# Kernel optimization log

Hardware: AMD Instinct MI355X
Metric: run time of the kernel (lower is better)

The kernel has to match this reference:

```python
import jax, jax.numpy as jnp
import numpy as np

J, H, MAXREL = 24, 8, 49  # num_joints, temporal heads, max_relative_position


def _pos_encoding(seq_len, d_model):
    pos = jnp.arange(seq_len, dtype=jnp.float32)[:, None]
    i = jnp.arange(d_model, dtype=jnp.float32)[None, :]
    angle = pos / jnp.power(10000.0, 2.0 * jnp.floor(i / 2.0) / d_model)
    return jnp.where(jnp.arange(d_model)[None, :] % 2 == 0, jnp.sin(angle), jnp.cos(angle))  # [S, D]


def _rel_index(seq_len):
    r = jnp.arange(seq_len)
    dist = jnp.clip(r[None, :] - r[:, None], -MAXREL, MAXREL) + MAXREL
    return dist  # [S, S] int


def setup_inputs() -> dict:
    key = jax.random.key(0)
    ks = jax.random.split(key, 12)
    B, S, D = 32, 120, 128
    depth = D // H
    s = 0.02
    x = jax.random.normal(ks[0], (B, S, J, D), dtype=jnp.float32)
    mask = jnp.triu(jnp.ones((1, 1, S, S), dtype=jnp.float32), k=1)  # look-ahead mask
    Wq = jax.random.normal(ks[1], (J, D, D), dtype=jnp.float32) * s
    bq = jnp.zeros((J, D), dtype=jnp.float32)
    Wk = jax.random.normal(ks[2], (J, D, D), dtype=jnp.float32) * s
    bk = jnp.zeros((J, D), dtype=jnp.float32)
    Wv = jax.random.normal(ks[3], (J, D, D), dtype=jnp.float32) * s
    bv = jnp.zeros((J, D), dtype=jnp.float32)
    Wo = jax.random.normal(ks[4], (D, D), dtype=jnp.float32) * s
    bo = jnp.zeros((D,), dtype=jnp.float32)
    key_table = jax.random.normal(ks[5], (2 * MAXREL + 1, depth), dtype=jnp.float32) * s
    val_table = jax.random.normal(ks[6], (2 * MAXREL + 1, depth), dtype=jnp.float32) * s
    return {"x": x, "mask": mask, "Wq": Wq, "bq": bq, "Wk": Wk, "bk": bk,
            "Wv": Wv, "bv": bv, "Wo": Wo, "bo": bo,
            "key_table": key_table, "val_table": val_table}


def reference(x, mask, Wq, bq, Wk, bk, Wv, bv, Wo, bo, key_table, val_table):
    B, S, _, D = x.shape
    depth = D // H
    # absolute positional encoding, broadcast over batch and joints
    x = x + _pos_encoding(S, D)[None, :, None, :]
    xj = jnp.transpose(x, (2, 0, 1, 3))  # [J, B, S, D]
    # per-joint linear projections (torch Linear: y = x @ W^T + b)
    q = jnp.einsum('jbsd,jed->jbse', xj, Wq) + bq[:, None, None, :]
    k = jnp.einsum('jbsd,jed->jbse', xj, Wk) + bk[:, None, None, :]
    v = jnp.einsum('jbsd,jed->jbse', xj, Wv) + bv[:, None, None, :]
    # split heads -> [J, B, H, S, depth]
    split = lambda t: t.reshape(J, B, S, H, depth).transpose(0, 1, 3, 2, 4)
    q, k, v = split(q), split(k), split(v)
    # relative key/value embeddings [S, S, depth]
    rel = _rel_index(S)
    rk = key_table[rel]
    rv = val_table[rel]
    logits = jnp.einsum('jbhsd,jbhtd->jbhst', q, k) + jnp.einsum('jbhsd,std->jbhst', q, rk)
    logits = logits / jnp.float32(np.sqrt(depth)) + mask * (-1e9)
    w = jax.nn.softmax(logits, axis=-1)  # [J, B, H, S, T]
    out = jnp.einsum('jbhst,jbhtd->jbhsd', w, v) + jnp.einsum('jbhst,std->jbhsd', w, rv)
    out = out.transpose(0, 1, 3, 2, 4).reshape(J, B, S, D)  # merge heads
    out = jnp.einsum('jbsd,ed->jbse', out, Wo) + bo  # shared output projection
    outputs = out.transpose(1, 2, 0, 3)  # [B, S, J, D]
    attn_weights = w[..., -1, :].transpose(1, 0, 2, 3)  # [B, J, H, T]
    return outputs, attn_weights
```

## Files before the change

kernel.cpp:

```cpp
#include <hip/hip_runtime.h>
#include <math.h>

#define Jn 24
#define Bn 32
#define Sn 120
#define Dn 128
#define Hn 8
#define DEP 16
#define JC 6
#define NCHUNK 4
#define ALD 136

typedef short bf16x8 __attribute__((ext_vector_type(8)));
typedef float f32x4 __attribute__((ext_vector_type(4)));

__device__ __forceinline__ unsigned short f2b(float f) {
    union { float f; unsigned u; } v; v.f = f;
    unsigned r = v.u + 0x7FFFu + ((v.u >> 16) & 1u);
    return (unsigned short)(r >> 16);
}
__device__ __forceinline__ float b2f(unsigned u16) {
    union { unsigned u; float f; } v; v.u = u16 << 16;
    return v.f;
}

__global__ void pe_kernel(float* __restrict__ pe) {
    const int s = blockIdx.x, d = threadIdx.x;
    const float expo = (float)(2 * (d >> 1)) / (float)Dn;
    const float base = powf(10000.0f, -expo);
    const float ang = (float)s * base;
    pe[s * Dn + d] = (d & 1) ? cosf(ang) : sinf(ang);
}

__global__ __launch_bounds__(256)
void qkv_gemm(const float* __restrict__ x, const float* __restrict__ pe,
              const float* __restrict__ Wq, const float* __restrict__ bq,
              const float* __restrict__ Wk, const float* __restrict__ bk,
              const float* __restrict__ Wv, const float* __restrict__ bv,
              unsigned short* __restrict__ qg, unsigned short* __restrict__ kg,
              unsigned short* __restrict__ vg, int jbase)
{
    extern __shared__ unsigned short lsu[];
    unsigned short* As = lsu;
    unsigned short* Bs = lsu + 128 * ALD;

    const int bid = blockIdx.x;
    const int nt = bid % 3;
    const int mt = (bid / 3) % 30;
    const int jc = bid / 90;
    const int j = jbase + jc;
    const int tid = threadIdx.x;

    const float* Wsel = (nt == 0 ? Wq : (nt == 1 ? Wk : Wv)) + (size_t)j * Dn * Dn;
    const float* bsel = (nt == 0 ? bq : (nt == 1 ? bk : bv)) + (size_t)j * Dn;
    unsigned short* obuf = (nt == 0 ? qg : (nt == 1 ? kg : vg));

    for (int idx = tid; idx < 128 * 32; idx += 256) {
        const int r = idx >> 5;
        const int c = (idx & 31) << 2;
        const int mflat = mt * 128 + r;
        const int b = mflat / Sn;
        const int s = mflat % Sn;
        const float4 xv = *(const float4*)(x + (((size_t)(b * Sn + s)) * Jn + j) * Dn + c);
        const float4 pv = *(const float4*)(pe + s * Dn + c);
        unsigned short* dst = As + r * ALD + c;
        dst[0] = f2b(xv.x + pv.x); dst[1] = f2b(xv.y + pv.y);
        dst[2] = f2b(xv.z + pv.z); dst[3] = f2b(xv.w + pv.w);
    }
    for (int idx = tid; idx < 128 * 32; idx += 256) {
        const int e = idx >> 5;
        const int c = (idx & 31) << 2;
        const float4 wv = *(const float4*)(Wsel + (size_t)e * Dn + c);
        unsigned short* dst = Bs + e * ALD + c;
        dst[0] = f2b(wv.x); dst[1] = f2b(wv.y); dst[2] = f2b(wv.z); dst[3] = f2b(wv.w);
    }
    __syncthreads();

    const int wid = tid >> 6;
    const int lane = tid & 63;
    const int wm = wid >> 1, wn = wid & 1;
    const int g = lane >> 4, q16 = lane & 15;

    f32x4 acc[4][4];
    #pragma unroll
    for (int a = 0; a < 4; ++a)
        #pragma unroll
        for (int c2 = 0; c2 < 4; ++c2) acc[a][c2] = (f32x4){0.f, 0.f, 0.f, 0.f};

    #pragma unroll
    for (int ks = 0; ks < 4; ++ks) {
        const int kof = ks * 32 + g * 8;
        bf16x8 av[4], bvf[4];
        #pragma unroll
        for (int fr = 0; fr < 4; ++fr)
            av[fr] = *(const bf16x8*)(As + (wm * 64 + fr * 16 + q16) * ALD + kof);
        #pragma unroll
        for (int fc = 0; fc < 4; ++fc)
            bvf[fc] = *(const bf16x8*)(Bs + (wn * 64 + fc * 16 + q16) * ALD + kof);
        #pragma unroll
        for (int fr = 0; fr < 4; ++fr)
            #pragma unroll
            for (int fc = 0; fc < 4; ++fc)
                acc[fr][fc] = __builtin_amdgcn_mfma_f32_16x16x32_bf16(av[fr], bvf[fc], acc[fr][fc], 0, 0, 0);
    }

    #pragma unroll
    for (int fc = 0; fc < 4; ++fc) {
        const int e = wn * 64 + fc * 16 + q16;
        const float be = bsel[e];
        const int h = e >> 4, ed = e & 15;
        #pragma unroll
        for (int fr = 0; fr < 4; ++fr) {
            #pragma unroll
            for (int r = 0; r < 4; ++r) {
                const int mflat = mt * 128 + wm * 64 + fr * 16 + g * 4 + r;
                const int b = mflat / Sn, s = mflat % Sn;
                obuf[((size_t)((jc * Bn + b) * Hn + h)) * (Sn * DEP) + s * DEP + ed] =
                    f2b(acc[fr][fc][r] + be);
            }
        }
    }
}

#define A_VCT  0
#define A_RKT  6400
#define A_ABUF 9472
#define A_QRB  35072
#define A_BYTES 43776

__global__ __launch_bounds__(256)
void attn_mfma(const unsigned short* __restrict__ qg, const unsigned short* __restrict__ kg,
               const unsigned short* __restrict__ vg,
               const float* __restrict__ ktab, const float* __restrict__ vtab,
               unsigned short* __restrict__ out_pre, float* __restrict__ attn_w, int jbase)
{
    extern __shared__ char smc[];
    unsigned short* vct = (unsigned short*)(smc + A_VCT);
    unsigned short* rkt = (unsigned short*)(smc + A_RKT);

    const int tid = threadIdx.x;
    const int wid = tid >> 6;
    const int lane = tid & 63;
    const int l15 = lane & 15;
    const int g = lane >> 4;
    const int bh = blockIdx.x;
    const int jc = bh >> 8;
    const int b = (bh >> 3) & 31;
    const int h = bh & 7;
    const int j = jbase + jc;

    unsigned short* ab = (unsigned short*)(smc + A_ABUF) + wid * 16 * 200;
    _Float16*      qrb = (_Float16*)(smc + A_QRB) + wid * 16 * 68;

    {
        unsigned* z = (unsigned*)smc;
        for (int idx = tid; idx < A_BYTES / 4; idx += 256) z[idx] = 0;
    }
    __syncthreads();
    const unsigned* vs = (const unsigned*)vg + (size_t)bh * 960;
    for (int idx = tid; idx < 960; idx += 256) {
        const int s = idx >> 3, ep = idx & 7;
        const unsigned u = vs[idx];
        vct[(2 * ep) * 200 + s] = (unsigned short)(u & 0xffffu);
        vct[(2 * ep + 1) * 200 + s] = (unsigned short)(u >> 16);
    }
    for (int idx = tid; idx < 800; idx += 256) {
        const int d = idx >> 4, e = idx & 15;
        vct[e * 200 + 128 + d] = f2b(vtab[d * DEP + e]);
    }
    for (int idx = tid; idx < 800; idx += 256) {
        const int d = idx >> 4, e = idx & 15;
        rkt[d * 24 + e] = f2b(ktab[d * DEP + e]);
    }
    __syncthreads();

    const unsigned short* qgu = qg + (size_t)bh * 1920;
    const unsigned short* kgu = kg + (size_t)bh * 1920;

    const bf16x8 zf = {0, 0, 0, 0, 0, 0, 0, 0};
    const f32x4 z4 = {0.f, 0.f, 0.f, 0.f};

    #pragma unroll
    for (int half = 0; half < 2; ++half) {
        const int m = half ? (7 - wid) : wid;

        const bf16x8 afr = (g < 2) ? *(const bf16x8*)(qgu + (16 * m + l15) * 16 + g * 8) : zf;
        f32x4 qr[4];
        #pragma unroll
        for (int n = 0; n < 4; ++n) {
            const bf16x8 bfr = (g < 2) ? *(const bf16x8*)(rkt + (16 * n + l15) * 24 + g * 8) : zf;
            qr[n] = __builtin_amdgcn_mfma_f32_16x16x32_bf16(afr, bfr, z4, 0, 0, 0);
        }
        f32x4 acc[8];
        #pragma unroll
        for (int n = 0; n < 8; ++n) {
            if (n > m) break;
            const bf16x8 bfr = (g < 2) ? *(const bf16x8*)(kgu + (16 * n + l15) * 16 + g * 8) : zf;
            acc[n] = __builtin_amdgcn_mfma_f32_16x16x32_bf16(afr, bfr, z4, 0, 0, 0);
        }
        #pragma unroll
        for (int n = 0; n < 4; ++n)
            #pragma unroll
            for (int r = 0; r < 4; ++r)
                qrb[(g * 4 + r) * 68 + 16 * n + l15] = (_Float16)qr[n][r];

        float rs[4];
        #pragma unroll
        for (int r = 0; r < 4; ++r) {
            const int srow = 16 * m + g * 4 + r;
            float pv[8];
            float tot = 0.f, far = 0.f;
            #pragma unroll
            for (int n = 0; n < 8; ++n) {
                if (n > m) break;
                const int t = 16 * n + l15;
                const int dd = t - srow;
                const int dist = (dd <= -49) ? 0 : dd + 49;
                const float qrv = (float)qrb[(g * 4 + r) * 68 + dist];
                float p = 0.f;
                if (t <= srow) p = __expf((acc[n][r] + qrv) * 0.25f);
                pv[n] = p;
                tot += p;
                if (dd <= -49) far += p;
            }
            #pragma unroll
            for (int mk = 1; mk < 16; mk <<= 1) {
                tot += __shfl_xor(tot, mk);
                far += __shfl_xor(far, mk);
            }
            rs[r] = tot;
            const float inv = 1.f / tot;
            #pragma unroll
            for (int n = 0; n < 8; ++n) {
                if (n > m) break;
                const int t = 16 * n + l15;
                const int dd = t - srow;
                ab[(g * 4 + r) * 200 + 16 * n + l15] = f2b(pv[n]);
                if (dd >= -48 && dd <= 0)
                    ab[(g * 4 + r) * 200 + 128 + dd + 49] = f2b(pv[n]);
                if (srow == Sn - 1 && t < Sn)
                    attn_w[(((size_t)(b * Jn + j)) * Hn + h) * Sn + t] = pv[n] * inv;
            }
            if (l15 == 0)
                ab[(g * 4 + r) * 200 + 128 + 0] = f2b(far);
        }

        f32x4 oacc = z4;
        #pragma unroll
        for (int kt = 0; kt < 4; ++kt) {
            if (kt > (m >> 1)) break;
            const bf16x8 aw = *(const bf16x8*)(ab + l15 * 200 + kt * 32 + g * 8);
            const bf16x8 bv = *(const bf16x8*)(vct + l15 * 200 + kt * 32 + g * 8);
            oacc = __builtin_amdgcn_mfma_f32_16x16x32_bf16(aw, bv, oacc, 0, 0, 0);
        }
        #pragma unroll
        for (int kt = 4; kt < 6; ++kt) {
            const bf16x8 aw = *(const bf16x8*)(ab + l15 * 200 + kt * 32 + g * 8);
            const bf16x8 bv = *(const bf16x8*)(vct + l15 * 200 + kt * 32 + g * 8);
            oacc = __builtin_amdgcn_mfma_f32_16x16x32_bf16(aw, bv, oacc, 0, 0, 0);
        }
        #pragma unroll
        for (int r = 0; r < 4; ++r) {
            const int srow = 16 * m + g * 4 + r;
            if (srow < Sn)
                out_pre[((size_t)((j * Bn + b) * Sn) + srow) * Dn + h * DEP + l15] =
                    f2b(oacc[r] / rs[r]);
        }
    }
}

__global__ __launch_bounds__(256)
void oproj_gemm(const unsigned short* __restrict__ Ain, const float* __restrict__ Wo,
                const float* __restrict__ bo, float* __restrict__ out)
{
    extern __shared__ unsigned short lsu[];
    unsigned short* As = lsu;
    unsigned short* Bs = lsu + 128 * ALD;
    const int tid = threadIdx.x;
    const int mt = blockIdx.x;

    for (int idx = tid; idx < 128 * 16; idx += 256) {
        const int r = idx >> 4;
        const int c = (idx & 15) << 3;
        *(uint4*)(As + r * ALD + c) = *(const uint4*)(Ain + ((size_t)(mt * 128 + r)) * Dn + c);
    }
    for (int idx = tid; idx < 128 * 32; idx += 256) {
        const int e = idx >> 5;
        const int c = (idx & 31) << 2;
        const float4 wv = *(const float4*)(Wo + (size_t)e * Dn + c);
        unsigned short* dst = Bs + e * ALD + c;
        dst[0] = f2b(wv.x); dst[1] = f2b(wv.y); dst[2] = f2b(wv.z); dst[3] = f2b(wv.w);
    }
    __syncthreads();

    const int wid = tid >> 6;
    const int lane = tid & 63;
    const int wm = wid >> 1, wn = wid & 1;
    const int g = lane >> 4, q16 = lane & 15;

    f32x4 acc[4][4];
    #pragma unroll
    for (int a = 0; a < 4; ++a)
        #pragma unroll
        for (int c2 = 0; c2 < 4; ++c2) acc[a][c2] = (f32x4){0.f, 0.f, 0.f, 0.f};

    #pragma unroll
    for (int ks = 0; ks < 4; ++ks) {
        const int kof = ks * 32 + g * 8;
        bf16x8 av[4], bvf[4];
        #pragma unroll
        for (int fr = 0; fr < 4; ++fr)
            av[fr] = *(const bf16x8*)(As + (wm * 64 + fr * 16 + q16) * ALD + kof);
        #pragma unroll
        for (int fc = 0; fc < 4; ++fc)
            bvf[fc] = *(const bf16x8*)(Bs + (wn * 64 + fc * 16 + q16) * ALD + kof);
        #pragma unroll
        for (int fr = 0; fr < 4; ++fr)
            #pragma unroll
            for (int fc = 0; fc < 4; ++fc)
                acc[fr][fc] = __builtin_amdgcn_mfma_f32_16x16x32_bf16(av[fr], bvf[fc], acc[fr][fc], 0, 0, 0);
    }

    #pragma unroll
    for (int fc = 0; fc < 4; ++fc) {
        const int e = wn * 64 + fc * 16 + q16;
        const float be = bo[e];
        #pragma unroll
        for (int fr = 0; fr < 4; ++fr) {
            #pragma unroll
            for (int r = 0; r < 4; ++r) {
                const int m = mt * 128 + wm * 64 + fr * 16 + g * 4 + r;
                const int jj = m / (Bn * Sn);
                const int rem = m % (Bn * Sn);
                const int bb = rem / Sn, ss = rem % Sn;
                out[((size_t)(bb * Sn + ss) * Jn + jj) * Dn + e] = acc[fr][fc][r] + be;
            }
        }
    }
}

extern "C" void kernel_launch(void* const* d_in, const int* in_sizes, int n_in,
                              void* d_out, int out_size, void* d_ws, size_t ws_size,
                              hipStream_t stream)
{
    const float* x    = (const float*)d_in[0];
    const float* Wq   = (const float*)d_in[2];
    const float* bq   = (const float*)d_in[3];
    const float* Wk   = (const float*)d_in[4];
    const float* bk   = (const float*)d_in[5];
    const float* Wv   = (const float*)d_in[6];
    const float* bv   = (const float*)d_in[7];
    const float* Wo   = (const float*)d_in[8];
    const float* bo   = (const float*)d_in[9];
    const float* ktab = (const float*)d_in[10];
    const float* vtab = (const float*)d_in[11];

    float* out    = (float*)d_out;
    float* attn_w = out + (size_t)Bn * Sn * Jn * Dn;

    float* pe = (float*)d_ws;
    char* base = (char*)d_ws;
    const size_t csz = (size_t)JC * Bn * Hn * Sn * DEP;
    unsigned short* qg = (unsigned short*)(base + 65536);
    unsigned short* kg = qg + csz;
    unsigned short* vg = kg + csz;
    unsigned short* out_pre = vg + csz;

    pe_kernel<<<Sn, Dn, 0, stream>>>(pe);
    const int gemm_lds = 2 * 128 * ALD * 2;
    for (int c = 0; c < NCHUNK; ++c) {
        qkv_gemm<<<JC * 30 * 3, 256, gemm_lds, stream>>>(
            x, pe, Wq, bq, Wk, bk, Wv, bv, qg, kg, vg, c * JC);
        attn_mfma<<<JC * Bn * Hn, 256, A_BYTES, stream>>>(
            qg, kg, vg, ktab, vtab, out_pre, attn_w, c * JC);
    }
    oproj_gemm<<<(Jn * Bn * Sn) / 128, 256, gemm_lds, stream>>>(out_pre, Wo, bo, out);
}
```

Measured before the change: 267.2 us.

## Reuse the x tile across Q/K/V, fold softmax scale into Q, single-chunk launch

The QKV GEMM now loads and converts each x tile once and loops over the three weight matrices, instead of launching three blocks that each reload it. Q is prescaled by log2(e)/sqrt(depth) so the softmax can use a raw exp2. The far-distance relative-value bucket is handled by subtracting table row 0 and adding it back after normalisation, which removes the 'far' sum and its shuffles. When the workspace is large enough, all 24 joints run in one qkv/attn launch pair instead of four chunks. The cost is that each GEMM block runs serially over three weights with extra barriers, and the larger Q/K/V buffers need more workspace.

```diff
diff --git a/kernel.cpp b/kernel.cpp
--- a/kernel.cpp
+++ b/kernel.cpp
@@ -7,12 +7,18 @@
 #define Dn 128
 #define Hn 8
 #define DEP 16
-#define JC 6
-#define NCHUNK 4
 #define ALD 136
+
+#define QSCL 0.36067376022224085f
 
 typedef short bf16x8 __attribute__((ext_vector_type(8)));
 typedef float f32x4 __attribute__((ext_vector_type(4)));
+
+#if __has_builtin(__builtin_amdgcn_exp2f)
+#define EXP2(x) __builtin_amdgcn_exp2f(x)
+#else
+#define EXP2(x) exp2f(x)
+#endif
 
 __device__ __forceinline__ unsigned short f2b(float f) {
     union { float f; unsigned u; } v; v.f = f;
@@ -45,15 +51,10 @@
     unsigned short* Bs = lsu + 128 * ALD;
 
     const int bid = blockIdx.x;
-    const int nt = bid % 3;
-    const int mt = (bid / 3) % 30;
-    const int jc = bid / 90;
+    const int mt = bid % 30;
+    const int jc = bid / 30;
     const int j = jbase + jc;
     const int tid = threadIdx.x;
-
-    const float* Wsel = (nt == 0 ? Wq : (nt == 1 ? Wk : Wv)) + (size_t)j * Dn * Dn;
-    const float* bsel = (nt == 0 ? bq : (nt == 1 ? bk : bv)) + (size_t)j * Dn;
-    unsigned short* obuf = (nt == 0 ? qg : (nt == 1 ? kg : vg));
 
     for (int idx = tid; idx < 128 * 32; idx += 256) {
         const int r = idx >> 5;
@@ -67,56 +68,65 @@
         dst[0] = f2b(xv.x + pv.x); dst[1] = f2b(xv.y + pv.y);
         dst[2] = f2b(xv.z + pv.z); dst[3] = f2b(xv.w + pv.w);
     }
-    for (int idx = tid; idx < 128 * 32; idx += 256) {
-        const int e = idx >> 5;
-        const int c = (idx & 31) << 2;
-        const float4 wv = *(const float4*)(Wsel + (size_t)e * Dn + c);
-        unsigned short* dst = Bs + e * ALD + c;
-        dst[0] = f2b(wv.x); dst[1] = f2b(wv.y); dst[2] = f2b(wv.z); dst[3] = f2b(wv.w);
-    }
-    __syncthreads();
 
     const int wid = tid >> 6;
     const int lane = tid & 63;
     const int wm = wid >> 1, wn = wid & 1;
     const int g = lane >> 4, q16 = lane & 15;
 
-    f32x4 acc[4][4];
-    #pragma unroll
-    for (int a = 0; a < 4; ++a)
-        #pragma unroll
-        for (int c2 = 0; c2 < 4; ++c2) acc[a][c2] = (f32x4){0.f, 0.f, 0.f, 0.f};
-
-    #pragma unroll
-    for (int ks = 0; ks < 4; ++ks) {
-        const int kof = ks * 32 + g * 8;
-        bf16x8 av[4], bvf[4];
-        #pragma unroll
-        for (int fr = 0; fr < 4; ++fr)
-            av[fr] = *(const bf16x8*)(As + (wm * 64 + fr * 16 + q16) * ALD + kof);
-        #pragma unroll
-        for (int fc = 0; fc < 4; ++fc)
-            bvf[fc] = *(const bf16x8*)(Bs + (wn * 64 + fc * 16 + q16) * ALD + kof);
-        #pragma unroll
-        for (int fr = 0; fr < 4; ++fr)
+    for (int nt = 0; nt < 3; ++nt) {
+        const float* Wsel = (nt == 0 ? Wq : (nt == 1 ? Wk : Wv)) + (size_t)j * Dn * Dn;
+        const float* bsel = (nt == 0 ? bq : (nt == 1 ? bk : bv)) + (size_t)j * Dn;
+        unsigned short* obuf = (nt == 0 ? qg : (nt == 1 ? kg : vg));
+        const float scl = (nt == 0) ? QSCL : 1.0f;
+
+        if (nt) __syncthreads();
+        for (int idx = tid; idx < 128 * 32; idx += 256) {
+            const int e = idx >> 5;
+            const int c = (idx & 31) << 2;
+            const float4 wv = *(const float4*)(Wsel + (size_t)e * Dn + c);
+            unsigned short* dst = Bs + e * ALD + c;
+            dst[0] = f2b(wv.x); dst[1] = f2b(wv.y); dst[2] = f2b(wv.z); dst[3] = f2b(wv.w);
+        }
+        __syncthreads();
+
+        f32x4 acc[4][4];
+        #pragma unroll
+        for (int a = 0; a < 4; ++a)
+            #pragma unroll
+            for (int c2 = 0; c2 < 4; ++c2) acc[a][c2] = (f32x4){0.f, 0.f, 0.f, 0.f};
+
+        #pragma unroll
+        for (int ks = 0; ks < 4; ++ks) {
+            const int kof = ks * 32 + g * 8;
+            bf16x8 av[4], bvf[4];
+            #pragma unroll
+            for (int fr = 0; fr < 4; ++fr)
+                av[fr] = *(const bf16x8*)(As + (wm * 64 + fr * 16 + q16) * ALD + kof);
             #pragma unroll
             for (int fc = 0; fc < 4; ++fc)
-                acc[fr][fc] = __builtin_amdgcn_mfma_f32_16x16x32_bf16(av[fr], bvf[fc], acc[fr][fc], 0, 0, 0);
-    }
-
-    #pragma unroll
-    for (int fc = 0; fc < 4; ++fc) {
-        const int e = wn * 64 + fc * 16 + q16;
-        const float be = bsel[e];
-        const int h = e >> 4, ed = e & 15;
-        #pragma unroll
-        for (int fr = 0; fr < 4; ++fr) {
-            #pragma unroll
-            for (int r = 0; r < 4; ++r) {
-                const int mflat = mt * 128 + wm * 64 + fr * 16 + g * 4 + r;
-                const int b = mflat / Sn, s = mflat % Sn;
-                obuf[((size_t)((jc * Bn + b) * Hn + h)) * (Sn * DEP) + s * DEP + ed] =
-                    f2b(acc[fr][fc][r] + be);
+                bvf[fc] = *(const bf16x8*)(Bs + (wn * 64 + fc * 16 + q16) * ALD + kof);
+            #pragma unroll
+            for (int fr = 0; fr < 4; ++fr)
+                #pragma unroll
+                for (int fc = 0; fc < 4; ++fc)
+                    acc[fr][fc] = __builtin_amdgcn_mfma_f32_16x16x32_bf16(av[fr], bvf[fc], acc[fr][fc], 0, 0, 0);
+        }
+
+        #pragma unroll
+        for (int fc = 0; fc < 4; ++fc) {
+            const int e = wn * 64 + fc * 16 + q16;
+            const float be = bsel[e];
+            const int h = e >> 4, ed = e & 15;
+            #pragma unroll
+            for (int fr = 0; fr < 4; ++fr) {
+                #pragma unroll
+                for (int r = 0; r < 4; ++r) {
+                    const int mflat = mt * 128 + wm * 64 + fr * 16 + g * 4 + r;
+                    const int b = mflat / Sn, s = mflat % Sn;
+                    obuf[((size_t)((jc * Bn + b) * Hn + h)) * (Sn * DEP) + s * DEP + ed] =
+                        f2b((acc[fr][fc][r] + be) * scl);
+                }
             }
         }
     }
@@ -124,9 +134,10 @@
 
 #define A_VCT  0
 #define A_RKT  6400
-#define A_ABUF 9472
-#define A_QRB  35072
-#define A_BYTES 43776
+#define A_RV0  9472
+#define A_ABUF 9536
+#define A_QRB  35136
+#define A_BYTES 43840
 
 __global__ __launch_bounds__(256)
 void attn_mfma(const unsigned short* __restrict__ qg, const unsigned short* __restrict__ kg,
@@ -137,6 +148,7 @@
     extern __shared__ char smc[];
     unsigned short* vct = (unsigned short*)(smc + A_VCT);
     unsigned short* rkt = (unsigned short*)(smc + A_RKT);
+    float*          rv0 = (float*)(smc + A_RV0);
 
     const int tid = threadIdx.x;
     const int wid = tid >> 6;
@@ -166,12 +178,13 @@
     }
     for (int idx = tid; idx < 800; idx += 256) {
         const int d = idx >> 4, e = idx & 15;
-        vct[e * 200 + 128 + d] = f2b(vtab[d * DEP + e]);
+        vct[e * 200 + 128 + d] = f2b(vtab[d * DEP + e] - vtab[e]);
     }
     for (int idx = tid; idx < 800; idx += 256) {
         const int d = idx >> 4, e = idx & 15;
         rkt[d * 24 + e] = f2b(ktab[d * DEP + e]);
     }
+    if (tid < 16) rv0[tid] = vtab[tid];
     __syncthreads();
 
     const unsigned short* qgu = qg + (size_t)bh * 1920;
@@ -179,6 +192,7 @@
 
     const bf16x8 zf = {0, 0, 0, 0, 0, 0, 0, 0};
     const f32x4 z4 = {0.f, 0.f, 0.f, 0.f};
+    const float rv0f = rv0[l15];
 
     #pragma unroll
     for (int half = 0; half < 2; ++half) {
@@ -209,7 +223,7 @@
         for (int r = 0; r < 4; ++r) {
             const int srow = 16 * m + g * 4 + r;
             float pv[8];
-            float tot = 0.f, far = 0.f;
+            float tot = 0.f;
             #pragma unroll
             for (int n = 0; n < 8; ++n) {
                 if (n > m) break;
@@ -218,31 +232,33 @@
                 const int dist = (dd <= -49) ? 0 : dd + 49;
                 const float qrv = (float)qrb[(g * 4 + r) * 68 + dist];
                 float p = 0.f;
-                if (t <= srow) p = __expf((acc[n][r] + qrv) * 0.25f);
+                if (t <= srow) p = EXP2(acc[n][r] + qrv);
                 pv[n] = p;
                 tot += p;
-                if (dd <= -49) far += p;
             }
             #pragma unroll
-            for (int mk = 1; mk < 16; mk <<= 1) {
-                tot += __shfl_xor(tot, mk);
-                far += __shfl_xor(far, mk);
-            }
+            for (int mk = 1; mk < 16; mk <<= 1) tot += __shfl_xor(tot, mk);
             rs[r] = tot;
-            const float inv = 1.f / tot;
             #pragma unroll
             for (int n = 0; n < 8; ++n) {
                 if (n > m) break;
                 const int t = 16 * n + l15;
                 const int dd = t - srow;
-                ab[(g * 4 + r) * 200 + 16 * n + l15] = f2b(pv[n]);
+                const unsigned short pb = f2b(pv[n]);
+                ab[(g * 4 + r) * 200 + t] = pb;
                 if (dd >= -48 && dd <= 0)
-                    ab[(g * 4 + r) * 200 + 128 + dd + 49] = f2b(pv[n]);
-                if (srow == Sn - 1 && t < Sn)
-                    attn_w[(((size_t)(b * Jn + j)) * Hn + h) * Sn + t] = pv[n] * inv;
+                    ab[(g * 4 + r) * 200 + 128 + dd + 49] = pb;
             }
-            if (l15 == 0)
-                ab[(g * 4 + r) * 200 + 128 + 0] = f2b(far);
+            if (srow == Sn - 1) {
+                const float inv = 1.f / tot;
+                #pragma unroll
+                for (int n = 0; n < 8; ++n) {
+                    if (n > m) break;
+                    const int t = 16 * n + l15;
+                    if (t < Sn)
+                        attn_w[(((size_t)(b * Jn + j)) * Hn + h) * Sn + t] = pv[n] * inv;
+                }
+            }
         }
 
         f32x4 oacc = z4;
@@ -264,7 +280,7 @@
             const int srow = 16 * m + g * 4 + r;
             if (srow < Sn)
                 out_pre[((size_t)((j * Bn + b) * Sn) + srow) * Dn + h * DEP + l15] =
-                    f2b(oacc[r] / rs[r]);
+                    f2b(oacc[r] / rs[r] + rv0f);
         }
     }
 }
@@ -358,9 +374,16 @@
     float* out    = (float*)d_out;
     float* attn_w = out + (size_t)Bn * Sn * Jn * Dn;
 
+    const size_t fullE = (size_t)Jn * Bn * Sn * Dn;
+    int JCr = 24;
+    {
+        const size_t need = 65536 + 2 * (3 * fullE + fullE);
+        if (ws_size < need) JCr = 6;
+    }
+    const size_t csz = (size_t)JCr * Bn * Hn * Sn * DEP;
+
     float* pe = (float*)d_ws;
     char* base = (char*)d_ws;
-    const size_t csz = (size_t)JC * Bn * Hn * Sn * DEP;
     unsigned short* qg = (unsigned short*)(base + 65536);
     unsigned short* kg = qg + csz;
     unsigned short* vg = kg + csz;
@@ -368,11 +391,11 @@
 
     pe_kernel<<<Sn, Dn, 0, stream>>>(pe);
     const int gemm_lds = 2 * 128 * ALD * 2;
-    for (int c = 0; c < NCHUNK; ++c) {
-        qkv_gemm<<<JC * 30 * 3, 256, gemm_lds, stream>>>(
-            x, pe, Wq, bq, Wk, bk, Wv, bv, qg, kg, vg, c * JC);
-        attn_mfma<<<JC * Bn * Hn, 256, A_BYTES, stream>>>(
-            qg, kg, vg, ktab, vtab, out_pre, attn_w, c * JC);
+    for (int c = 0; c < Jn; c += JCr) {
+        qkv_gemm<<<JCr * 30, 256, gemm_lds, stream>>>(
+            x, pe, Wq, bq, Wk, bk, Wv, bv, qg, kg, vg, c);
+        attn_mfma<<<JCr * Bn * Hn, 256, A_BYTES, stream>>>(
+            qg, kg, vg, ktab, vtab, out_pre, attn_w, c);
     }
     oproj_gemm<<<(Jn * Bn * Sn) / 128, 256, gemm_lds, stream>>>(out_pre, Wo, bo, out);
 }
```

Result: faster. 224.0 us (-16.2%).
